# Kernel optimization log

Hardware: AMD Instinct MI355X
Metric: run time of the kernel (lower is better)

Reference implementation:

```python
import jax, jax.numpy as jnp
import numpy as np


def _conv1x1(x, w, b):
    # x: [B,C,H,W], w: [O,C], b: [O]  (1x1 conv == per-pixel matmul)
    return jnp.einsum('bchw,oc->bohw', x, w) + b[None, :, None, None]


def setup_inputs() -> dict:
    key = jax.random.key(0)
    ks = jax.random.split(key, 9)
    B, C, H, W = 4, 64, 64, 64
    Ch = C // 2
    s_in = 1.0 / np.sqrt(C)
    s_h = 1.0 / np.sqrt(Ch)
    return {
        'x': jax.random.normal(ks[0], (B, C, H, W), dtype=jnp.float32),
        'w1': jax.random.normal(ks[1], (Ch, C), dtype=jnp.float32) * s_in,
        'b1': jax.random.normal(ks[2], (Ch,), dtype=jnp.float32) * s_in,
        'w2': jax.random.normal(ks[3], (Ch, C), dtype=jnp.float32) * s_in,
        'b2': jax.random.normal(ks[4], (Ch,), dtype=jnp.float32) * s_in,
        'w3': jax.random.normal(ks[5], (Ch, C), dtype=jnp.float32) * s_in,
        'b3': jax.random.normal(ks[6], (Ch,), dtype=jnp.float32) * s_in,
        'w4': jax.random.normal(ks[7], (C, Ch), dtype=jnp.float32) * s_h,
        'b4': jax.random.normal(ks[8], (C,), dtype=jnp.float32) * s_h,
    }


def reference(x, w1, b1, w2, b2, w3, b3, w4, b4):
    B, C, H, W = x.shape
    N = H * W
    # NOTE: original torch code does .view (raw reshape) with NO permute,
    # so channel/spatial axes get mixed exactly as in the source.
    x1 = _conv1x1(x, w1, b1).reshape(B, N, -1)   # [B, N, C/2] (raw reshape)
    x2 = _conv1x1(x, w2, b2).reshape(B, -1, N)   # [B, C/2, N]
    attn = jnp.matmul(x1, x2)                    # [B, N, N]
    # F.softmax with no dim on a 3D tensor -> legacy implicit dim = 0 (batch)
    attn = jax.nn.softmax(attn, axis=0)
    y = _conv1x1(x, w3, b3).reshape(B, N, -1)    # [B, N, C/2]
    y = jnp.matmul(attn, y)                      # [B, N, C/2]
    y = y.reshape(B, -1, H, W)                   # [B, C/2, H, W]
    return _conv1x1(y, w4, b4)                   # [B, C, H, W]
```

## Files before the change

### kernel.cpp

```cpp
#include <hip/hip_runtime.h>


typedef _Float16 half8 __attribute__((ext_vector_type(8)));
typedef float f32x4 __attribute__((ext_vector_type(4)));

#define N_PIX 4096
#define CIN   64
#define CHD   32
#define NB    4
#define JS    4


__global__ __launch_bounds__(256) void convs_kernel(
    const float* __restrict__ x,
    const float* __restrict__ w1, const float* __restrict__ b1,
    const float* __restrict__ w2, const float* __restrict__ b2,
    const float* __restrict__ w3, const float* __restrict__ b3,
    _Float16* __restrict__ X1h, _Float16* __restrict__ X2t, _Float16* __restrict__ Y3t)
{
    const int t = blockIdx.y;
    const float* w  = (t == 0) ? w1 : ((t == 1) ? w2 : w3);
    const float* bb = (t == 0) ? b1 : ((t == 1) ? b2 : b3);

    __shared__ float sw[CHD][CIN];
    __shared__ float sbias[CHD];
    __shared__ _Float16 sT[32 * 264];
    const int tid = threadIdx.x;
    for (int e = tid; e < CHD * CIN; e += 256) sw[e >> 6][e & 63] = w[e];
    if (tid < CHD) sbias[tid] = bb[tid];
    __syncthreads();

    const int b  = blockIdx.x >> 4;
    const int hw = ((blockIdx.x & 15) << 8) + tid;

    float xi[CIN];
    const float* xb = x + b * CIN * N_PIX + hw;
    #pragma unroll
    for (int c = 0; c < CIN; c++) xi[c] = xb[c * N_PIX];

    float out[CHD];
    for (int o = 0; o < CHD; o++) {
        float a0 = sbias[o], a1 = 0.f, a2 = 0.f, a3 = 0.f;
        #pragma unroll
        for (int c = 0; c < CIN; c += 4) {
            a0 += xi[c + 0] * sw[o][c + 0];
            a1 += xi[c + 1] * sw[o][c + 1];
            a2 += xi[c + 2] * sw[o][c + 2];
            a3 += xi[c + 3] * sw[o][c + 3];
        }
        out[o] = (a0 + a1) + (a2 + a3);
    }

    if (t == 0) {
        #pragma unroll
        for (int o = 0; o < CHD; o++)
            X1h[b * 131072 + o * N_PIX + hw] = (_Float16)out[o];
    } else if (t == 1) {
        #pragma unroll
        for (int mc = 0; mc < 4; mc++) {
            half8 v;
            #pragma unroll
            for (int e = 0; e < 8; e++) v[e] = (_Float16)out[mc * 8 + e];
            *(half8*)&X2t[b * 131072 + hw * 32 + mc * 8] = v;
        }
    } else {
        const int c  = tid & 31;
        const int jl = tid >> 5;
        #pragma unroll
        for (int o = 0; o < CHD; o++)
            sT[c * 264 + o * 8 + jl] = (_Float16)out[o];
        __syncthreads();
        const int jb0 = (blockIdx.x & 15) << 3;
        #pragma unroll
        for (int g = 0; g < 4; g++) {
            int u  = g * 256 + tid;
            int c2 = (u >> 5) & 31;
            int o2 = u & 31;
            half8 v = *(half8*)&sT[c2 * 264 + o2 * 8];
            *(half8*)&Y3t[b * 131072 + c2 * 4096 + o2 * 128 + jb0] = v;
        }
    }
}

__global__ __launch_bounds__(256) void attn_kernel(
    const _Float16* __restrict__ X1h, const _Float16* __restrict__ X2t,
    const _Float16* __restrict__ Y3t, float* __restrict__ OP)
{
    __shared__ float sRed[4 * 64 * 64];

    const int tid  = threadIdx.x;
    const int wv   = tid >> 6;
    const int lane = tid & 63;
    const int m    = lane & 15;
    const int q    = lane >> 4;
    const int ip   = blockIdx.x;
    const int js   = blockIdx.y;
    const int i0   = ip * 32;
    const int jbase = js * 1024 + wv * 256;

    half8 bx1[NB][2];
    #pragma unroll
    for (int b = 0; b < NB; b++)
        #pragma unroll
        for (int il = 0; il < 2; il++)
            bx1[b][il] = *(const half8*)&X1h[b * 131072 + (i0 + il * 16 + m) * 32 + q * 8];

    f32x4 oaccT[NB][2][2];
    #pragma unroll
    for (int b = 0; b < NB; b++)
        #pragma unroll
        for (int ch = 0; ch < 2; ch++)
            #pragma unroll
            for (int il = 0; il < 2; il++)
                oaccT[b][ch][il] = (f32x4){0.f, 0.f, 0.f, 0.f};

    const int jrow0 = ((m >> 2) * 8) + (m & 3);

    #pragma unroll 2
    for (int jt = 0; jt < 8; jt++) {
        const int j0 = jbase + jt * 32;

        half8 ax2[NB][2], ay3[NB][2];
        #pragma unroll
        for (int b = 0; b < NB; b++) {
            #pragma unroll
            for (int jh = 0; jh < 2; jh++)
                ax2[b][jh] = *(const half8*)&X2t[b * 131072 + (j0 + jrow0 + jh * 4) * 32 + q * 8];
            #pragma unroll
            for (int ch = 0; ch < 2; ch++)
                ay3[b][ch] = *(const half8*)&Y3t[b * 131072 + (ch * 16 + m) * 4096 + j0 + q * 8];
        }

        #pragma unroll
        for (int il = 0; il < 2; il++) {
            f32x4 sT[NB][2];
            #pragma unroll
            for (int b = 0; b < NB; b++)
                #pragma unroll
                for (int jh = 0; jh < 2; jh++)
                    sT[b][jh] = __builtin_amdgcn_mfma_f32_16x16x32_f16(
                        ax2[b][jh], bx1[b][il], (f32x4){0.f, 0.f, 0.f, 0.f}, 0, 0, 0);

            half8 pf[NB];
            #pragma unroll
            for (int jh = 0; jh < 2; jh++)
                #pragma unroll
                for (int r = 0; r < 4; r++) {
                    float s0 = sT[0][jh][r], s1 = sT[1][jh][r];
                    float s2 = sT[2][jh][r], s3 = sT[3][jh][r];
                    float mx = fmaxf(fmaxf(s0, s1), fmaxf(s2, s3));
                    float e0 = __expf(s0 - mx), e1 = __expf(s1 - mx);
                    float e2 = __expf(s2 - mx), e3 = __expf(s3 - mx);
                    float rs = 1.0f / (e0 + e1 + e2 + e3);
                    pf[0][jh * 4 + r] = (_Float16)(e0 * rs);
                    pf[1][jh * 4 + r] = (_Float16)(e1 * rs);
                    pf[2][jh * 4 + r] = (_Float16)(e2 * rs);
                    pf[3][jh * 4 + r] = (_Float16)(e3 * rs);
                }

            #pragma unroll
            for (int b = 0; b < NB; b++)
                #pragma unroll
                for (int ch = 0; ch < 2; ch++)
                    oaccT[b][ch][il] = __builtin_amdgcn_mfma_f32_16x16x32_f16(
                        ay3[b][ch], pf[b], oaccT[b][ch][il], 0, 0, 0);
        }
    }

    #pragma unroll
    for (int b = 0; b < NB; b++)
        #pragma unroll
        for (int ch = 0; ch < 2; ch++)
            #pragma unroll
            for (int il = 0; il < 2; il++)
                #pragma unroll
                for (int r = 0; r < 4; r++)
                    sRed[(wv * 64 + b * 16 + ch * 8 + il * 4 + r) * 64 + lane] =
                        oaccT[b][ch][il][r];
    __syncthreads();

    const int br = wv;
    float* op = OP + js * 524288 + (br * 4096 + i0) * 32;
    #pragma unroll
    for (int ch = 0; ch < 2; ch++)
        #pragma unroll
        for (int il = 0; il < 2; il++) {
            f32x4 v;
            #pragma unroll
            for (int r = 0; r < 4; r++) {
                int f = br * 16 + ch * 8 + il * 4 + r;
                v[r] = sRed[(0 * 64 + f) * 64 + lane] + sRed[(1 * 64 + f) * 64 + lane]
                     + sRed[(2 * 64 + f) * 64 + lane] + sRed[(3 * 64 + f) * 64 + lane];
            }
            *(f32x4*)&op[(il * 16 + m) * 32 + ch * 16 + q * 4] = v;
        }
}

__global__ __launch_bounds__(256) void out_kernel(
    const float* __restrict__ OP, const float* __restrict__ w4,
    const float* __restrict__ b4, float* __restrict__ out)
{
    __shared__ float sw[CIN][CHD];
    __shared__ float sbias[CIN];
    const int tid = threadIdx.x;
    for (int e = tid; e < CIN * CHD; e += 256) sw[e >> 5][e & 31] = w4[e];
    if (tid < CIN) sbias[tid] = b4[tid];
    __syncthreads();

    const int b  = blockIdx.x >> 4;
    const int hw = ((blockIdx.x & 15) << 8) + tid;
    const int o0 = blockIdx.y * 32;

    float y2[CHD];
    #pragma unroll
    for (int ch = 0; ch < CHD; ch++) {
        float v = 0.f;
        #pragma unroll
        for (int p = 0; p < JS; p++)
            v += OP[p * 524288 + b * 131072 + ch * 4096 + hw];
        y2[ch] = v;
    }

    float* ob = out + b * CIN * N_PIX + hw;
    for (int o = o0; o < o0 + 32; o++) {
        float a0 = sbias[o], a1 = 0.f, a2 = 0.f, a3 = 0.f;
        #pragma unroll
        for (int c = 0; c < CHD; c += 4) {
            a0 += y2[c + 0] * sw[o][c + 0];
            a1 += y2[c + 1] * sw[o][c + 1];
            a2 += y2[c + 2] * sw[o][c + 2];
            a3 += y2[c + 3] * sw[o][c + 3];
        }
        ob[o * N_PIX] = (a0 + a1) + (a2 + a3);
    }
}

extern "C" void kernel_launch(void* const* d_in, const int* in_sizes, int n_in,
                              void* d_out, int out_size, void* d_ws, size_t ws_size,
                              hipStream_t stream) {
    const float* x  = (const float*)d_in[0];
    const float* w1 = (const float*)d_in[1];
    const float* b1 = (const float*)d_in[2];
    const float* w2 = (const float*)d_in[3];
    const float* b2 = (const float*)d_in[4];
    const float* w3 = (const float*)d_in[5];
    const float* b3 = (const float*)d_in[6];
    const float* w4 = (const float*)d_in[7];
    const float* b4 = (const float*)d_in[8];

    char* wsb = (char*)d_ws;
    _Float16* X1h = (_Float16*)(wsb);
    _Float16* X2t = (_Float16*)(wsb + (1 << 20));
    _Float16* Y3t = (_Float16*)(wsb + (2 << 20));
    float*    OP  = (float*)   (wsb + (3 << 20));
    float*    out = (float*)d_out;

    dim3 g1(64, 3);
    convs_kernel<<<g1, 256, 0, stream>>>(x, w1, b1, w2, b2, w3, b3, X1h, X2t, Y3t);
    dim3 g2(128, JS);
    attn_kernel<<<g2, 256, 0, stream>>>(X1h, X2t, Y3t, OP);
    dim3 g3(64, 2);
    out_kernel<<<g3, 256, 0, stream>>>(OP, w4, b4, out);
}
```

Measured before the change: 145.6 us.

## Halve per-block work in all kernels to double grid size and read weights directly

```diff
diff --git a/kernel.cpp b/kernel.cpp
--- a/kernel.cpp
+++ b/kernel.cpp
@@ -5,8 +5,6 @@
 typedef float f32x4 __attribute__((ext_vector_type(4)));
 
 #define N_PIX 4096
-#define CIN   64
-#define CHD   32
 #define NB    4
 #define JS    4
 
@@ -19,65 +17,65 @@
     _Float16* __restrict__ X1h, _Float16* __restrict__ X2t, _Float16* __restrict__ Y3t)
 {
     const int t = blockIdx.y;
-    const float* w  = (t == 0) ? w1 : ((t == 1) ? w2 : w3);
-    const float* bb = (t == 0) ? b1 : ((t == 1) ? b2 : b3);
-
-    __shared__ float sw[CHD][CIN];
-    __shared__ float sbias[CHD];
-    __shared__ _Float16 sT[32 * 264];
-    const int tid = threadIdx.x;
-    for (int e = tid; e < CHD * CIN; e += 256) sw[e >> 6][e & 63] = w[e];
-    if (tid < CHD) sbias[tid] = bb[tid];
-    __syncthreads();
-
-    const int b  = blockIdx.x >> 4;
-    const int hw = ((blockIdx.x & 15) << 8) + tid;
-
-    float xi[CIN];
-    const float* xb = x + b * CIN * N_PIX + hw;
-    #pragma unroll
-    for (int c = 0; c < CIN; c++) xi[c] = xb[c * N_PIX];
-
-    float out[CHD];
-    for (int o = 0; o < CHD; o++) {
-        float a0 = sbias[o], a1 = 0.f, a2 = 0.f, a3 = 0.f;
-        #pragma unroll
-        for (int c = 0; c < CIN; c += 4) {
-            a0 += xi[c + 0] * sw[o][c + 0];
-            a1 += xi[c + 1] * sw[o][c + 1];
-            a2 += xi[c + 2] * sw[o][c + 2];
-            a3 += xi[c + 3] * sw[o][c + 3];
-        }
-        out[o] = (a0 + a1) + (a2 + a3);
+    const float* __restrict__ w  = (t == 0) ? w1 : ((t == 1) ? w2 : w3);
+    const float* __restrict__ bb = (t == 0) ? b1 : ((t == 1) ? b2 : b3);
+
+    __shared__ _Float16 sT[32 * 132];
+
+    const int tid   = threadIdx.x;
+    const int b     = blockIdx.x >> 5;
+    const int chunk = (blockIdx.x >> 1) & 15;
+    const int oh    = blockIdx.x & 1;
+    const int o0    = oh * 16;
+    const int hw    = chunk * 256 + tid;
+
+    float xi[64];
+    const float* xb = x + b * 64 * N_PIX + hw;
+    #pragma unroll
+    for (int c = 0; c < 64; c++) xi[c] = xb[c * N_PIX];
+
+    float acc[16];
+    #pragma unroll
+    for (int oo = 0; oo < 16; oo++) {
+        const int o = o0 + oo;
+        float a0 = bb[o], a1 = 0.f, a2 = 0.f, a3 = 0.f;
+        #pragma unroll
+        for (int c = 0; c < 64; c += 4) {
+            a0 += xi[c + 0] * w[o * 64 + c + 0];
+            a1 += xi[c + 1] * w[o * 64 + c + 1];
+            a2 += xi[c + 2] * w[o * 64 + c + 2];
+            a3 += xi[c + 3] * w[o * 64 + c + 3];
+        }
+        acc[oo] = (a0 + a1) + (a2 + a3);
     }
 
     if (t == 0) {
         #pragma unroll
-        for (int o = 0; o < CHD; o++)
-            X1h[b * 131072 + o * N_PIX + hw] = (_Float16)out[o];
+        for (int oo = 0; oo < 16; oo++)
+            X1h[b * 131072 + (o0 + oo) * N_PIX + hw] = (_Float16)acc[oo];
     } else if (t == 1) {
         #pragma unroll
-        for (int mc = 0; mc < 4; mc++) {
+        for (int mc = 0; mc < 2; mc++) {
             half8 v;
             #pragma unroll
-            for (int e = 0; e < 8; e++) v[e] = (_Float16)out[mc * 8 + e];
-            *(half8*)&X2t[b * 131072 + hw * 32 + mc * 8] = v;
+            for (int e = 0; e < 8; e++) v[e] = (_Float16)acc[mc * 8 + e];
+            *(half8*)&X2t[b * 131072 + hw * 32 + o0 + mc * 8] = v;
         }
     } else {
         const int c  = tid & 31;
         const int jl = tid >> 5;
         #pragma unroll
-        for (int o = 0; o < CHD; o++)
-            sT[c * 264 + o * 8 + jl] = (_Float16)out[o];
+        for (int oo = 0; oo < 16; oo++)
+            sT[c * 132 + oo * 8 + jl] = (_Float16)acc[oo];
         __syncthreads();
-        const int jb0 = (blockIdx.x & 15) << 3;
-        #pragma unroll
-        for (int g = 0; g < 4; g++) {
-            int u  = g * 256 + tid;
-            int c2 = (u >> 5) & 31;
-            int o2 = u & 31;
-            half8 v = *(half8*)&sT[c2 * 264 + o2 * 8];
-            *(half8*)&Y3t[b * 131072 + c2 * 4096 + o2 * 128 + jb0] = v;
+        const int jb0 = chunk * 8;
+        #pragma unroll
+        for (int g = 0; g < 2; g++) {
+            int u   = g * 256 + tid;
+            int c2  = u & 31;
+            int oo2 = u >> 5;
+            half8 v = *(half8*)&sT[c2 * 132 + oo2 * 8];
+            *(half8*)&Y3t[b * 131072 + c2 * 4096 + (o0 + oo2) * 128 + jb0] = v;
         }
     }
 }
@@ -86,37 +84,31 @@
     const _Float16* __restrict__ X1h, const _Float16* __restrict__ X2t,
     const _Float16* __restrict__ Y3t, float* __restrict__ OP)
 {
-    __shared__ float sRed[4 * 64 * 64];
+    __shared__ float sRed[4 * 32 * 64];
 
     const int tid  = threadIdx.x;
     const int wv   = tid >> 6;
     const int lane = tid & 63;
     const int m    = lane & 15;
     const int q    = lane >> 4;
-    const int ip   = blockIdx.x;
+    const int i0   = blockIdx.x * 16;
     const int js   = blockIdx.y;
-    const int i0   = ip * 32;
     const int jbase = js * 1024 + wv * 256;
 
-    half8 bx1[NB][2];
+    half8 bx1[NB];
     #pragma unroll
     for (int b = 0; b < NB; b++)
-        #pragma unroll
-        for (int il = 0; il < 2; il++)
-            bx1[b][il] = *(const half8*)&X1h[b * 131072 + (i0 + il * 16 + m) * 32 + q * 8];
-
-    f32x4 oaccT[NB][2][2];
-    #pragma unroll
-    for (int b = 0; b < NB; b++)
-        #pragma unroll
-        for (int ch = 0; ch < 2; ch++)
-            #pragma unroll
-            for (int il = 0; il < 2; il++)
-                oaccT[b][ch][il] = (f32x4){0.f, 0.f, 0.f, 0.f};
+        bx1[b] = *(const half8*)&X1h[b * 131072 + (i0 + m) * 32 + q * 8];
+
+    f32x4 oaccT[NB][2];
+    #pragma unroll
+    for (int b = 0; b < NB; b++) {
+        oaccT[b][0] = (f32x4){0.f, 0.f, 0.f, 0.f};
+        oaccT[b][1] = (f32x4){0.f, 0.f, 0.f, 0.f};
+    }
 
     const int jrow0 = ((m >> 2) * 8) + (m & 3);
 
-    #pragma unroll 2
     for (int jt = 0; jt < 8; jt++) {
         const int j0 = jbase + jt * 32;
 
@@ -131,40 +123,37 @@
                 ay3[b][ch] = *(const half8*)&Y3t[b * 131072 + (ch * 16 + m) * 4096 + j0 + q * 8];
         }
 
-        #pragma unroll
-        for (int il = 0; il < 2; il++) {
-            f32x4 sT[NB][2];
-            #pragma unroll
-            for (int b = 0; b < NB; b++)
-                #pragma unroll
-                for (int jh = 0; jh < 2; jh++)
-                    sT[b][jh] = __builtin_amdgcn_mfma_f32_16x16x32_f16(
-                        ax2[b][jh], bx1[b][il], (f32x4){0.f, 0.f, 0.f, 0.f}, 0, 0, 0);
-
-            half8 pf[NB];
+        f32x4 sT[NB][2];
+        #pragma unroll
+        for (int b = 0; b < NB; b++)
             #pragma unroll
             for (int jh = 0; jh < 2; jh++)
-                #pragma unroll
-                for (int r = 0; r < 4; r++) {
-                    float s0 = sT[0][jh][r], s1 = sT[1][jh][r];
-                    float s2 = sT[2][jh][r], s3 = sT[3][jh][r];
-                    float mx = fmaxf(fmaxf(s0, s1), fmaxf(s2, s3));
-                    float e0 = __expf(s0 - mx), e1 = __expf(s1 - mx);
-                    float e2 = __expf(s2 - mx), e3 = __expf(s3 - mx);
-                    float rs = 1.0f / (e0 + e1 + e2 + e3);
-                    pf[0][jh * 4 + r] = (_Float16)(e0 * rs);
-                    pf[1][jh * 4 + r] = (_Float16)(e1 * rs);
-                    pf[2][jh * 4 + r] = (_Float16)(e2 * rs);
-                    pf[3][jh * 4 + r] = (_Float16)(e3 * rs);
-                }
-
-            #pragma unroll
-            for (int b = 0; b < NB; b++)
-                #pragma unroll
-                for (int ch = 0; ch < 2; ch++)
-                    oaccT[b][ch][il] = __builtin_amdgcn_mfma_f32_16x16x32_f16(
-                        ay3[b][ch], pf[b], oaccT[b][ch][il], 0, 0, 0);
-        }
+                sT[b][jh] = __builtin_amdgcn_mfma_f32_16x16x32_f16(
+                    ax2[b][jh], bx1[b], (f32x4){0.f, 0.f, 0.f, 0.f}, 0, 0, 0);
+
+        half8 pf[NB];
+        #pragma unroll
+        for (int jh = 0; jh < 2; jh++)
+            #pragma unroll
+            for (int r = 0; r < 4; r++) {
+                float s0 = sT[0][jh][r], s1 = sT[1][jh][r];
+                float s2 = sT[2][jh][r], s3 = sT[3][jh][r];
+                float mx = fmaxf(fmaxf(s0, s1), fmaxf(s2, s3));
+                float e0 = __expf(s0 - mx), e1 = __expf(s1 - mx);
+                float e2 = __expf(s2 - mx), e3 = __expf(s3 - mx);
+                float rs = __builtin_amdgcn_rcpf(e0 + e1 + e2 + e3);
+                pf[0][jh * 4 + r] = (_Float16)(e0 * rs);
+                pf[1][jh * 4 + r] = (_Float16)(e1 * rs);
+                pf[2][jh * 4 + r] = (_Float16)(e2 * rs);
+                pf[3][jh * 4 + r] = (_Float16)(e3 * rs);
+            }
+
+        #pragma unroll
+        for (int b = 0; b < NB; b++)
+            #pragma unroll
+            for (int ch = 0; ch < 2; ch++)
+                oaccT[b][ch] = __builtin_amdgcn_mfma_f32_16x16x32_f16(
+                    ay3[b][ch], pf[b], oaccT[b][ch], 0, 0, 0);
     }
 
     #pragma unroll
@@ -172,48 +161,37 @@
         #pragma unroll
         for (int ch = 0; ch < 2; ch++)
             #pragma unroll
-            for (int il = 0; il < 2; il++)
-                #pragma unroll
-                for (int r = 0; r < 4; r++)
-                    sRed[(wv * 64 + b * 16 + ch * 8 + il * 4 + r) * 64 + lane] =
-                        oaccT[b][ch][il][r];
+            for (int r = 0; r < 4; r++)
+                sRed[(wv * 32 + b * 8 + ch * 4 + r) * 64 + lane] = oaccT[b][ch][r];
     __syncthreads();
 
     const int br = wv;
     float* op = OP + js * 524288 + (br * 4096 + i0) * 32;
     #pragma unroll
-    for (int ch = 0; ch < 2; ch++)
-        #pragma unroll
-        for (int il = 0; il < 2; il++) {
-            f32x4 v;
-            #pragma unroll
-            for (int r = 0; r < 4; r++) {
-                int f = br * 16 + ch * 8 + il * 4 + r;
-                v[r] = sRed[(0 * 64 + f) * 64 + lane] + sRed[(1 * 64 + f) * 64 + lane]
-                     + sRed[(2 * 64 + f) * 64 + lane] + sRed[(3 * 64 + f) * 64 + lane];
-            }
-            *(f32x4*)&op[(il * 16 + m) * 32 + ch * 16 + q * 4] = v;
-        }
+    for (int ch = 0; ch < 2; ch++) {
+        f32x4 v;
+        #pragma unroll
+        for (int r = 0; r < 4; r++) {
+            int f = br * 8 + ch * 4 + r;
+            v[r] = sRed[(0 * 32 + f) * 64 + lane] + sRed[(1 * 32 + f) * 64 + lane]
+                 + sRed[(2 * 32 + f) * 64 + lane] + sRed[(3 * 32 + f) * 64 + lane];
+        }
+        *(f32x4*)&op[m * 32 + ch * 16 + q * 4] = v;
+    }
 }
 
 __global__ __launch_bounds__(256) void out_kernel(
     const float* __restrict__ OP, const float* __restrict__ w4,
     const float* __restrict__ b4, float* __restrict__ out)
 {
-    __shared__ float sw[CIN][CHD];
-    __shared__ float sbias[CIN];
     const int tid = threadIdx.x;
-    for (int e = tid; e < CIN * CHD; e += 256) sw[e >> 5][e & 31] = w4[e];
-    if (tid < CIN) sbias[tid] = b4[tid];
-    __syncthreads();
-
-    const int b  = blockIdx.x >> 4;
-    const int hw = ((blockIdx.x & 15) << 8) + tid;
-    const int o0 = blockIdx.y * 32;
-
-    float y2[CHD];
-    #pragma unroll
-    for (int ch = 0; ch < CHD; ch++) {
+    const int b   = blockIdx.x >> 4;
+    const int hw  = ((blockIdx.x & 15) << 8) + tid;
+    const int o0  = blockIdx.y * 16;
+
+    float y2[32];
+    #pragma unroll
+    for (int ch = 0; ch < 32; ch++) {
         float v = 0.f;
         #pragma unroll
         for (int p = 0; p < JS; p++)
@@ -221,15 +199,17 @@
         y2[ch] = v;
     }
 
-    float* ob = out + b * CIN * N_PIX + hw;
-    for (int o = o0; o < o0 + 32; o++) {
-        float a0 = sbias[o], a1 = 0.f, a2 = 0.f, a3 = 0.f;
-        #pragma unroll
-        for (int c = 0; c < CHD; c += 4) {
-            a0 += y2[c + 0] * sw[o][c + 0];
-            a1 += y2[c + 1] * sw[o][c + 1];
-            a2 += y2[c + 2] * sw[o][c + 2];
-            a3 += y2[c + 3] * sw[o][c + 3];
+    float* ob = out + b * 64 * N_PIX + hw;
+    #pragma unroll
+    for (int oo = 0; oo < 16; oo++) {
+        const int o = o0 + oo;
+        float a0 = b4[o], a1 = 0.f, a2 = 0.f, a3 = 0.f;
+        #pragma unroll
+        for (int c = 0; c < 32; c += 4) {
+            a0 += y2[c + 0] * w4[o * 32 + c + 0];
+            a1 += y2[c + 1] * w4[o * 32 + c + 1];
+            a2 += y2[c + 2] * w4[o * 32 + c + 2];
+            a3 += y2[c + 3] * w4[o * 32 + c + 3];
         }
         ob[o * N_PIX] = (a0 + a1) + (a2 + a3);
     }
@@ -255,10 +235,10 @@
     float*    OP  = (float*)   (wsb + (3 << 20));
     float*    out = (float*)d_out;
 
-    dim3 g1(64, 3);
+    dim3 g1(128, 3);
     convs_kernel<<<g1, 256, 0, stream>>>(x, w1, b1, w2, b2, w3, b3, X1h, X2t, Y3t);
-    dim3 g2(128, JS);
+    dim3 g2(256, JS);
     attn_kernel<<<g2, 256, 0, stream>>>(X1h, X2t, Y3t, OP);
-    dim3 g3(64, 2);
+    dim3 g3(64, 4);
     out_kernel<<<g3, 256, 0, stream>>>(OP, w4, b4, out);
 }
```

After: 166.7 us. 14.5% more time.
